# Kernel tuning notes

Hardware: AMD Instinct MI355X
Metric: run time of the kernel (lower is better)

The kernel has to match this reference:

```python
import jax, jax.numpy as jnp
import numpy as np
from jax import lax

# static config matching init_kwargs
H, W = 128, 128
THETA_RES, RHO_RES = 1.0, 1.0
C_IN, C_OUT = 64, 64
A = int(np.round(180.0 / THETA_RES))            # num angle bins = 180
R = int(np.ceil(np.sqrt(H * H + W * W) / RHO_RES))  # num rho bins = 182


def _make_rho_idx():
    # rho bin index for every (angle, pixel); pixels flattened h-major (h*W + w)
    th = np.arange(A, dtype=np.float64) * THETA_RES * np.pi / 180.0
    hh, ww = np.meshgrid(np.arange(H), np.arange(W), indexing='ij')
    xs = (ww - W / 2.0).ravel()
    ys = (hh - H / 2.0).ravel()
    r = np.round((xs[None, :] * np.cos(th)[:, None]
                  + ys[None, :] * np.sin(th)[:, None]) / RHO_RES).astype(np.int32)
    r = r + R // 2
    return np.clip(r, 0, R - 1)  # [A, H*W] int32


def dht(x, rho_idx):
    # Hough scatter: [N,C,H,W] -> [N,C,A,R]
    N, C, h, w = x.shape
    xf = x.reshape(N * C, h * w).T  # [HW, NC]

    def step(_, idx_a):
        acc = jax.ops.segment_sum(xf, idx_a, num_segments=R)  # [R, NC]
        return None, acc

    _, ht = lax.scan(step, None, rho_idx)       # [A, R, NC]
    return ht.transpose(2, 0, 1).reshape(N, C, A, R)


def idht(ht, rho_idx):
    # inverse Hough gather (transpose of dht): [N,C,A,R] -> [N,C,H,W]
    N, C, a, r = ht.shape
    hf = ht.reshape(N * C, a, r).transpose(1, 0, 2)  # [A, NC, R]

    def step(acc, args):
        ht_a, idx_a = args
        return acc + ht_a[:, idx_a], None  # gather along rho -> [NC, HW]

    acc0 = jnp.zeros((N * C, H * W), ht.dtype)
    acc, _ = lax.scan(step, acc0, (hf, rho_idx))
    return acc.reshape(N, C, H, W)


def conv91_relu(x, w, b, groups):
    # Conv2d kernel (9,1), padding (4,0), stride 1 + ReLU
    y = lax.conv_general_dilated(x, w, (1, 1), [(4, 4), (0, 0)],
                                 dimension_numbers=('NCHW', 'OIHW', 'NCHW'),
                                 feature_group_count=groups)
    return jax.nn.relu(y + b[None, :, None, None])


def setup_inputs():
    key = jax.random.key(0)
    ks = jax.random.split(key, 7)
    N = 4
    x = jax.random.normal(ks[0], (N, C_IN, H, W), dtype=jnp.float32)
    s1 = 1.0 / np.sqrt(9.0)
    s2 = 1.0 / np.sqrt(9.0 * C_IN)
    w1 = jax.random.normal(ks[1], (C_IN, 1, 9, 1), jnp.float32) * s1
    b1 = jax.random.normal(ks[2], (C_IN,), jnp.float32) * 0.01
    w2 = jax.random.normal(ks[3], (C_IN, C_IN, 9, 1), jnp.float32) * s2
    b2 = jax.random.normal(ks[4], (C_IN,), jnp.float32) * 0.01
    w3 = jax.random.normal(ks[5], (C_OUT, C_IN, 9, 1), jnp.float32) * s2
    b3 = jax.random.normal(ks[6], (C_OUT,), jnp.float32) * 0.01
    rho_idx = jnp.asarray(_make_rho_idx())  # [A, H*W] int32, precomputed buffer
    return {"x": x, "rho_idx": rho_idx, "w1": w1, "b1": b1,
            "w2": w2, "b2": b2, "w3": w3, "b3": b3}


def reference(x, rho_idx, w1, b1, w2, b2, w3, b3):
    out = dht(x, rho_idx)                       # [N,C,A,R]
    out = conv91_relu(out, w1, b1, groups=C_IN) # grouped (9,1) conv
    out = conv91_relu(out, w2, b2, groups=1)
    out = conv91_relu(out, w3, b3, groups=1)
    return idht(out, rho_idx)                   # [N,C_OUT,H,W]
```

## Files before the change

kernel.cpp:

```cpp
#include <hip/hip_runtime.h>

typedef unsigned short ushort_t;
typedef __attribute__((ext_vector_type(8))) short short8;
typedef __attribute__((ext_vector_type(4))) float float4v;

#define HW 16384
#define A_BINS 180
#define R_BINS 182
#define AP 188
#define CCH 64
#define NB 4
#define NC 256
#define MROWS (A_BINS * R_BINS)
#define MPROWS (AP * R_BINS)

static __device__ __forceinline__ float b2f(ushort_t u) {
    union { unsigned u32; float f; } c; c.u32 = ((unsigned)u) << 16; return c.f;
}
static __device__ __forceinline__ float u2f(unsigned u) {
    union { unsigned u32; float f; } c; c.u32 = u; return c.f;
}
static __device__ __forceinline__ ushort_t f2b(float f) {
    union { float f; unsigned u; } c; c.f = f;
    unsigned r = c.u + 0x7fffu + ((c.u >> 16) & 1u);
    return (ushort_t)(r >> 16);
}
static __device__ __forceinline__ float4v cvt4(uint2 u) {
    return (float4v){u2f(u.x << 16), u2f(u.x & 0xffff0000u),
                     u2f(u.y << 16), u2f(u.y & 0xffff0000u)};
}

__global__ __launch_bounds__(256) void k_transpose(const float* __restrict__ x,
                                                   ushort_t* __restrict__ xT) {
    __shared__ float tile[64][65];
    int t = threadIdx.x, lane = t & 63, g = t >> 6;
    int pBase = blockIdx.x * 64;
    int ncBase = blockIdx.y * 64;
#pragma unroll
    for (int i = 0; i < 16; ++i) {
        int ncl = g + i * 4;
        tile[ncl][lane] = x[(size_t)(ncBase + ncl) * HW + pBase + lane];
    }
    __syncthreads();
#pragma unroll
    for (int i = 0; i < 16; ++i) {
        int pl = g + i * 4;
        xT[(size_t)(pBase + pl) * 256 + ncBase + lane] = f2b(tile[lane][pl]);
    }
}

__global__ __launch_bounds__(256) void k_setup(ushort_t* __restrict__ ht0,
                                               ushort_t* __restrict__ bufA,
                                               ushort_t* __restrict__ bufB,
                                               const float* __restrict__ w2,
                                               const float* __restrict__ w3,
                                               ushort_t* __restrict__ w2b,
                                               ushort_t* __restrict__ w3b) {
    int blk = blockIdx.x, t = threadIdx.x;
    if (blk < 24) {
        int b = blk >> 3, j = blk & 7;
        int ap = (j < 4) ? j : (184 + (j - 4));
        ushort_t* base = (b == 0 ? ht0 : (b == 1 ? bufA : bufB));
        uint4* p = (uint4*)(base + (size_t)ap * (R_BINS * NC));
        int n16 = R_BINS * NC / 8;
        for (int i = t; i < n16; i += 256) p[i] = (uint4){0, 0, 0, 0};
        return;
    }
    int rep = blk - 24;
    const float* w = (rep >= 144) ? w3 : w2;
    ushort_t* wb = (rep >= 144) ? w3b : w2b;
    int idx = (rep % 144) * 256 + t;
    int j = idx & 7;
    int lane = (idx >> 3) & 63;
    int cot = (idx >> 9) & 3;
    int h = (idx >> 11) & 1;
    int k = idx >> 12;
    int co = cot * 16 + (lane & 15);
    int ci = h * 32 + (lane >> 4) * 8 + j;
    wb[idx] = f2b(w[(co * 64 + ci) * 9 + k]);
}

__global__ __launch_bounds__(256) void k_csr(const int* __restrict__ rho,
                                             int* __restrict__ offs,
                                             ushort_t* __restrict__ plist) {
    __shared__ int hist[4][R_BINS];
    __shared__ int tot[R_BINS];
    __shared__ int offl[R_BINS + 1];
    __shared__ int cur[4][R_BINS];
    __shared__ ushort_t sp[HW];
    int a = blockIdx.x, t = threadIdx.x, lane = t & 63, wv = t >> 6;
    for (int i = t; i < 4 * R_BINS; i += 256) ((int*)hist)[i] = 0;
    __syncthreads();
    const int* rA = rho + (size_t)a * HW;
#pragma unroll 4
    for (int i = 0; i < 64; ++i) {
        int r = rA[t + i * 256];
        atomicAdd(&hist[wv][r], 1);
    }
    __syncthreads();
    if (t < R_BINS) tot[t] = hist[0][t] + hist[1][t] + hist[2][t] + hist[3][t];
    __syncthreads();
    if (wv == 0) {
        int b0 = lane * 3;
        int c0 = (b0     < R_BINS) ? tot[b0]     : 0;
        int c1 = (b0 + 1 < R_BINS) ? tot[b0 + 1] : 0;
        int c2 = (b0 + 2 < R_BINS) ? tot[b0 + 2] : 0;
        int sum = c0 + c1 + c2, inc = sum;
#pragma unroll
        for (int d = 1; d < 64; d <<= 1) {
            int vv = __shfl_up(inc, d);
            if (lane >= d) inc += vv;
        }
        int excl = inc - sum;
        if (b0     < R_BINS) offl[b0]     = excl;
        if (b0 + 1 < R_BINS) offl[b0 + 1] = excl + c0;
        if (b0 + 2 < R_BINS) offl[b0 + 2] = excl + c0 + c1;
        if (lane == 63) offl[R_BINS] = inc;
    }
    __syncthreads();
    if (t < R_BINS) {
        int b = offl[t];
        cur[0][t] = b; b += hist[0][t];
        cur[1][t] = b; b += hist[1][t];
        cur[2][t] = b; b += hist[2][t];
        cur[3][t] = b;
    }
    if (t <= R_BINS) offs[a * (R_BINS + 1) + t] = offl[t];
    __syncthreads();
#pragma unroll 4
    for (int i = 0; i < 64; ++i) {
        int p = t + i * 256;
        int r = rA[p];
        int pos = atomicAdd(&cur[wv][r], 1);
        sp[pos] = (ushort_t)p;
    }
    __syncthreads();
    const uint4* spv = (const uint4*)sp;
    uint4* plv = (uint4*)(plist + (size_t)a * HW);
    for (int i = t; i < HW / 8; i += 256) plv[i] = spv[i];
}

__global__ __launch_bounds__(256, 4) void k_dht_g4(const ushort_t* __restrict__ xT,
                                                   const int* __restrict__ offs,
                                                   const ushort_t* __restrict__ plist,
                                                   ushort_t* __restrict__ ht0) {
    int ax = blockIdx.x;
    int a = ax >> 1, half = ax & 1;
    int part = blockIdx.y;
    int t = threadIdx.x, lane = t & 63, wv = t >> 6;
    int wslot = part * 4 + wv;
    int lh = lane & 31;
    bool lowhalf = (lane < 32);
    int lh4 = lh * 4;
    const ushort_t* xh = xT + half * 128;
    const uint*  plw = (const uint*)(plist + (size_t)a * HW);
    const uint4* plq = (const uint4*)plw;
    const int* offA = offs + a * (R_BINS + 1);
    size_t obase = (size_t)(a + 4) * (R_BINS * NC) + half * 128;
    for (int r = wslot; r < R_BINS; r += 64) {
        int off = __builtin_amdgcn_readfirstlane(offA[r]);
        int end = __builtin_amdgcn_readfirstlane(offA[r + 1]);
        float4v acc = (float4v){0.f, 0.f, 0.f, 0.f};
        int j = off;
        if (j < end && (j & 1)) {
            unsigned up = __builtin_amdgcn_readfirstlane(plw[j >> 1]);
            unsigned p = up >> 16;
            uint2 u = *(const uint2*)(xh + (size_t)p * 256 + lh4);
            if (lowhalf) acc += cvt4(u);
            ++j;
        }
        while (j + 2 <= end && (j & 7)) {
            unsigned w = __builtin_amdgcn_readfirstlane(plw[j >> 1]);
            unsigned pe = w & 0xffffu, po = w >> 16;
            unsigned ps = lowhalf ? pe : po;
            uint2 u = *(const uint2*)(xh + (size_t)ps * 256 + lh4);
            acc += cvt4(u);
            j += 2;
        }
        if (j + 16 <= end) {
            uint4 q0 = plq[j >> 3];
            uint4 q1 = plq[(j >> 3) + 1];
            for (; j + 16 <= end; ) {
                int jn = j + 16;
                uint4 n0, n1;
                bool more = (jn + 16 <= end);
                if (more) {
                    n0 = plq[jn >> 3];
                    n1 = plq[(jn >> 3) + 1];
                }
                unsigned w0 = __builtin_amdgcn_readfirstlane(q0.x);
                unsigned w1 = __builtin_amdgcn_readfirstlane(q0.y);
                unsigned w2 = __builtin_amdgcn_readfirstlane(q0.z);
                unsigned w3 = __builtin_amdgcn_readfirstlane(q0.w);
                unsigned w4 = __builtin_amdgcn_readfirstlane(q1.x);
                unsigned w5 = __builtin_amdgcn_readfirstlane(q1.y);
                unsigned w6 = __builtin_amdgcn_readfirstlane(q1.z);
                unsigned w7 = __builtin_amdgcn_readfirstlane(q1.w);
                unsigned s0 = lowhalf ? (w0 & 0xffffu) : (w0 >> 16);
                unsigned s1 = lowhalf ? (w1 & 0xffffu) : (w1 >> 16);
                unsigned s2 = lowhalf ? (w2 & 0xffffu) : (w2 >> 16);
                unsigned s3 = lowhalf ? (w3 & 0xffffu) : (w3 >> 16);
                unsigned s4 = lowhalf ? (w4 & 0xffffu) : (w4 >> 16);
                unsigned s5 = lowhalf ? (w5 & 0xffffu) : (w5 >> 16);
                unsigned s6 = lowhalf ? (w6 & 0xffffu) : (w6 >> 16);
                unsigned s7 = lowhalf ? (w7 & 0xffffu) : (w7 >> 16);
                uint2 u0 = *(const uint2*)(xh + (size_t)s0 * 256 + lh4);
                uint2 u1 = *(const uint2*)(xh + (size_t)s1 * 256 + lh4);
                uint2 u2 = *(const uint2*)(xh + (size_t)s2 * 256 + lh4);
                uint2 u3 = *(const uint2*)(xh + (size_t)s3 * 256 + lh4);
                uint2 u4 = *(const uint2*)(xh + (size_t)s4 * 256 + lh4);
                uint2 u5 = *(const uint2*)(xh + (size_t)s5 * 256 + lh4);
                uint2 u6 = *(const uint2*)(xh + (size_t)s6 * 256 + lh4);
                uint2 u7 = *(const uint2*)(xh + (size_t)s7 * 256 + lh4);
                acc += cvt4(u0); acc += cvt4(u1); acc += cvt4(u2); acc += cvt4(u3);
                acc += cvt4(u4); acc += cvt4(u5); acc += cvt4(u6); acc += cvt4(u7);
                q0 = n0; q1 = n1; j = jn;
            }
        }
        for (; j + 8 <= end; j += 8) {
            uint4 q = plq[j >> 3];
            unsigned w0 = __builtin_amdgcn_readfirstlane(q.x);
            unsigned w1 = __builtin_amdgcn_readfirstlane(q.y);
            unsigned w2 = __builtin_amdgcn_readfirstlane(q.z);
            unsigned w3 = __builtin_amdgcn_readfirstlane(q.w);
            unsigned s0 = lowhalf ? (w0 & 0xffffu) : (w0 >> 16);
            unsigned s1 = lowhalf ? (w1 & 0xffffu) : (w1 >> 16);
            unsigned s2 = lowhalf ? (w2 & 0xffffu) : (w2 >> 16);
            unsigned s3 = lowhalf ? (w3 & 0xffffu) : (w3 >> 16);
            uint2 u0 = *(const uint2*)(xh + (size_t)s0 * 256 + lh4);
            uint2 u1 = *(const uint2*)(xh + (size_t)s1 * 256 + lh4);
            uint2 u2 = *(const uint2*)(xh + (size_t)s2 * 256 + lh4);
            uint2 u3 = *(const uint2*)(xh + (size_t)s3 * 256 + lh4);
            acc += cvt4(u0); acc += cvt4(u1); acc += cvt4(u2); acc += cvt4(u3);
        }
        while (j + 2 <= end) {
            unsigned w = __builtin_amdgcn_readfirstlane(plw[j >> 1]);
            unsigned pe = w & 0xffffu, po = w >> 16;
            unsigned ps = lowhalf ? pe : po;
            uint2 u = *(const uint2*)(xh + (size_t)ps * 256 + lh4);
            acc += cvt4(u);
            j += 2;
        }
        if (j < end) {
            unsigned up = __builtin_amdgcn_readfirstlane(plw[j >> 1]);
            unsigned p = up & 0xffffu;
            uint2 u = *(const uint2*)(xh + (size_t)p * 256 + lh4);
            if (lowhalf) acc += cvt4(u);
        }
        float4v oth;
        oth.x = __shfl(acc.x, lane ^ 32);
        oth.y = __shfl(acc.y, lane ^ 32);
        oth.z = __shfl(acc.z, lane ^ 32);
        oth.w = __shfl(acc.w, lane ^ 32);
        acc += oth;
        if (lowhalf) {
            unsigned lo = (unsigned)f2b(acc.x) | ((unsigned)f2b(acc.y) << 16);
            unsigned hi = (unsigned)f2b(acc.z) | ((unsigned)f2b(acc.w) << 16);
            *(uint2*)(ht0 + obase + (size_t)r * NC + lh4) = (uint2){lo, hi};
        }
    }
}

__global__ __launch_bounds__(256) void k_conv1(const ushort_t* __restrict__ ht0,
                                               const float* __restrict__ w1,
                                               const float* __restrict__ b1,
                                               ushort_t* __restrict__ bufA) {
    int t = threadIdx.x, c = t & 63;
    int r = blockIdx.x;
    int a0 = blockIdx.y * 30;
    float wr[9];
#pragma unroll
    for (int k = 0; k < 9; ++k) wr[k] = w1[c * 9 + k];
    float bb = b1[c];
    const ushort_t* ip = ht0 + ((size_t)a0 * R_BINS + r) * NC + t;
    float v[38];
#pragma unroll
    for (int j = 0; j < 38; ++j) v[j] = b2f(ip[(size_t)j * (R_BINS * NC)]);
    ushort_t* op = bufA + ((size_t)(a0 + 4) * R_BINS + r) * NC + t;
#pragma unroll
    for (int i = 0; i < 30; ++i) {
        float s = bb;
#pragma unroll
        for (int k = 0; k < 9; ++k) s = fmaf(v[i + k], wr[k], s);
        op[(size_t)i * (R_BINS * NC)] = f2b(fmaxf(s, 0.f));
    }
}

__global__ __launch_bounds__(256) void k_gemm(const ushort_t* __restrict__ in,
                                              const ushort_t* __restrict__ wb,
                                              const float* __restrict__ bias,
                                              ushort_t* __restrict__ out,
                                              int outRowOff) {
    __shared__ ushort_t Bs[36864];
    int t = threadIdx.x, lane = t & 63, wv = t >> 6;
    {
        const uint4* src = (const uint4*)wb;
        uint4* dst = (uint4*)Bs;
        for (int i = t; i < 36864 / 8; i += 256) dst[i] = src[i];
    }
    __syncthreads();
    int m = lane & 15, q = lane >> 4;
    int n = blockIdx.y;
    int rowBase = blockIdx.x * 256 + wv * 64;
    const ushort_t* inN = in + n * 64;
    size_t rof[4];
#pragma unroll
    for (int tl = 0; tl < 4; ++tl) {
        int row = rowBase + tl * 16 + m;
        int rowc = row < MROWS ? row : (MROWS - 1);
        rof[tl] = (size_t)rowc * NC;
    }
    float4v acc[4][4];
#pragma unroll
    for (int tl = 0; tl < 4; ++tl)
#pragma unroll
        for (int i = 0; i < 4; ++i) acc[tl][i] = (float4v){0.f, 0.f, 0.f, 0.f};

#pragma unroll
    for (int k = 0; k < 9; ++k) {
#pragma unroll
        for (int h = 0; h < 2; ++h) {
            const ushort_t* base = inN + (size_t)k * (R_BINS * NC) + h * 32 + q * 8;
            short8 af0 = *(const short8*)(base + rof[0]);
            short8 af1 = *(const short8*)(base + rof[1]);
            short8 af2 = *(const short8*)(base + rof[2]);
            short8 af3 = *(const short8*)(base + rof[3]);
            const ushort_t* bl = Bs + (size_t)((k * 2 + h) * 4) * 512 + lane * 8;
            short8 b0 = *(const short8*)(bl);
            short8 b1v = *(const short8*)(bl + 512);
            short8 b2v = *(const short8*)(bl + 1024);
            short8 b3v = *(const short8*)(bl + 1536);
            acc[0][0] = __builtin_amdgcn_mfma_f32_16x16x32_bf16(af0, b0, acc[0][0], 0, 0, 0);
            acc[0][1] = __builtin_amdgcn_mfma_f32_16x16x32_bf16(af0, b1v, acc[0][1], 0, 0, 0);
            acc[0][2] = __builtin_amdgcn_mfma_f32_16x16x32_bf16(af0, b2v, acc[0][2], 0, 0, 0);
            acc[0][3] = __builtin_amdgcn_mfma_f32_16x16x32_bf16(af0, b3v, acc[0][3], 0, 0, 0);
            acc[1][0] = __builtin_amdgcn_mfma_f32_16x16x32_bf16(af1, b0, acc[1][0], 0, 0, 0);
            acc[1][1] = __builtin_amdgcn_mfma_f32_16x16x32_bf16(af1, b1v, acc[1][1], 0, 0, 0);
            acc[1][2] = __builtin_amdgcn_mfma_f32_16x16x32_bf16(af1, b2v, acc[1][2], 0, 0, 0);
            acc[1][3] = __builtin_amdgcn_mfma_f32_16x16x32_bf16(af1, b3v, acc[1][3], 0, 0, 0);
            acc[2][0] = __builtin_amdgcn_mfma_f32_16x16x32_bf16(af2, b0, acc[2][0], 0, 0, 0);
            acc[2][1] = __builtin_amdgcn_mfma_f32_16x16x32_bf16(af2, b1v, acc[2][1], 0, 0, 0);
            acc[2][2] = __builtin_amdgcn_mfma_f32_16x16x32_bf16(af2, b2v, acc[2][2], 0, 0, 0);
            acc[2][3] = __builtin_amdgcn_mfma_f32_16x16x32_bf16(af2, b3v, acc[2][3], 0, 0, 0);
            acc[3][0] = __builtin_amdgcn_mfma_f32_16x16x32_bf16(af3, b0, acc[3][0], 0, 0, 0);
            acc[3][1] = __builtin_amdgcn_mfma_f32_16x16x32_bf16(af3, b1v, acc[3][1], 0, 0, 0);
            acc[3][2] = __builtin_amdgcn_mfma_f32_16x16x32_bf16(af3, b2v, acc[3][2], 0, 0, 0);
            acc[3][3] = __builtin_amdgcn_mfma_f32_16x16x32_bf16(af3, b3v, acc[3][3], 0, 0, 0);
        }
    }

    ushort_t* outN = out + n * 64;
#pragma unroll
    for (int tl = 0; tl < 4; ++tl) {
#pragma unroll
        for (int cot = 0; cot < 4; ++cot) {
            int co = cot * 16 + m;
            float bv = bias[co];
#pragma unroll
            for (int i = 0; i < 4; ++i) {
                int rowD = rowBase + tl * 16 + q * 4 + i;
                float v = fmaxf(acc[tl][cot][i] + bv, 0.f);
                if (rowD < MROWS) outN[(size_t)(rowD + outRowOff) * NC + co] = f2b(v);
            }
        }
    }
}

union SharedIdht {
    int rhoL[A_BINS * 32];
    float tile[2 * 256 * 33];
};

#define IDHT_LOAD(S, ang) do { \
    int4 rv0_ = *(const int4*)&u.rhoL[(ang) * 32 + wq * 8]; \
    int4 rv1_ = *(const int4*)&u.rhoL[(ang) * 32 + wq * 8 + 4]; \
    int rrs_[8] = {rv0_.x, rv0_.y, rv0_.z, rv0_.w, rv1_.x, rv1_.y, rv1_.z, rv1_.w}; \
    const ushort_t* bA_ = buf3 + (size_t)(ang) * (R_BINS * NC); \
    _Pragma("unroll") \
    for (int i_ = 0; i_ < 8; ++i_) { \
        int r_ = __builtin_amdgcn_readfirstlane(rrs_[i_]); \
        S[i_] = *(const uint2*)(bA_ + (size_t)r_ * NC + lo4); \
    } } while (0)

#define IDHT_CONSUME(S) do { \
    _Pragma("unroll") \
    for (int i_ = 0; i_ < 8; ++i_) accv[i_] += cvt4(S[i_]); \
    } while (0)

__global__ __launch_bounds__(512, 2) void k_idht(const ushort_t* __restrict__ buf3,
                                                 const int* __restrict__ rho,
                                                 float* __restrict__ outp) {
    __shared__ SharedIdht u;
    int t = threadIdx.x, lane = t & 63, wv = t >> 6;
    int grp = wv >> 2;
    int wq = wv & 3;
    int P0 = blockIdx.x * 32;
    int lo4 = lane << 2;
    for (int i = t; i < A_BINS * 32; i += 512) {
        int a = i >> 5, px = i & 31;
        u.rhoL[a * 32 + px] = rho[(size_t)a * HW + P0 + px];
    }
    __syncthreads();
    float4v accv[8];
#pragma unroll
    for (int i = 0; i < 8; ++i) accv[i] = (float4v){0.f, 0.f, 0.f, 0.f};
    int a0 = grp * 90;

    uint2 S0[8], S1[8], S2[8];
    IDHT_LOAD(S0, a0);
    IDHT_LOAD(S1, a0 + 1);
    IDHT_LOAD(S2, a0 + 2);
    for (int k = 0; k <= 84; k += 3) {
        IDHT_CONSUME(S0); IDHT_LOAD(S0, a0 + k + 3);
        IDHT_CONSUME(S1); IDHT_LOAD(S1, a0 + k + 4);
        IDHT_CONSUME(S2); IDHT_LOAD(S2, a0 + k + 5);
    }
    IDHT_CONSUME(S0);
    IDHT_CONSUME(S1);
    IDHT_CONSUME(S2);

    __syncthreads();
#pragma unroll
    for (int i = 0; i < 8; ++i) {
        int px = wq * 8 + i;
#pragma unroll
        for (int c = 0; c < 4; ++c)
            u.tile[(size_t)grp * 8448 + (lane * 4 + c) * 33 + px] = accv[i][c];
    }
    __syncthreads();
    int px = t & 31, nc0 = t >> 5;
    float* on = outp + P0 + px;
#pragma unroll
    for (int k = 0; k < 16; ++k) {
        int nc = nc0 + k * 16;
        on[(size_t)nc * HW] = u.tile[nc * 33 + px] + u.tile[8448 + nc * 33 + px];
    }
}

extern "C" void kernel_launch(void* const* d_in, const int* in_sizes, int n_in,
                              void* d_out, int out_size, void* d_ws, size_t ws_size,
                              hipStream_t stream) {
    const float* x   = (const float*)d_in[0];
    const int*   rho = (const int*)d_in[1];
    const float* w1  = (const float*)d_in[2];
    const float* b1  = (const float*)d_in[3];
    const float* w2  = (const float*)d_in[4];
    const float* b2  = (const float*)d_in[5];
    const float* w3  = (const float*)d_in[6];
    const float* b3  = (const float*)d_in[7];
    float* outp = (float*)d_out;

    char* ws = (char*)d_ws;
    size_t off = 0;
    auto alloc = [&](size_t bytes) -> void* {
        void* p = ws + off;
        off = (off + bytes + 255) & ~(size_t)255;
        return p;
    };
    ushort_t* xT    = (ushort_t*)alloc((size_t)HW * NC * 2);
    ushort_t* ht0   = (ushort_t*)alloc((size_t)AP * R_BINS * NC * 2);
    ushort_t* bufA  = (ushort_t*)alloc((size_t)AP * R_BINS * NC * 2);
    ushort_t* bufB  = (ushort_t*)alloc((size_t)AP * R_BINS * NC * 2);
    ushort_t* buf3  = (ushort_t*)alloc((size_t)A_BINS * R_BINS * NC * 2);
    ushort_t* w2b   = (ushort_t*)alloc(36864 * 2);
    ushort_t* w3b   = (ushort_t*)alloc(36864 * 2);
    int*      offs  = (int*)alloc((size_t)A_BINS * (R_BINS + 1) * 4);
    ushort_t* plist = (ushort_t*)alloc((size_t)A_BINS * HW * 2);

    k_transpose<<<dim3(256, 4), 256, 0, stream>>>(x, xT);
    k_setup<<<312, 256, 0, stream>>>(ht0, bufA, bufB, w2, w3, w2b, w3b);
    k_csr<<<A_BINS, 256, 0, stream>>>(rho, offs, plist);
    k_dht_g4<<<dim3(360, 16), 256, 0, stream>>>(xT, offs, plist, ht0);
    k_conv1<<<dim3(R_BINS, 6), 256, 0, stream>>>(ht0, w1, b1, bufA);
    k_gemm<<<dim3(128, NB), 256, 0, stream>>>(bufA, w2b, b2, bufB, 728);
    k_gemm<<<dim3(128, NB), 256, 0, stream>>>(bufB, w3b, b3, buf3, 0);
    k_idht<<<dim3(512), 512, 0, stream>>>(buf3, rho, outp);
}
```

Measured before the change: 371.5 us.

## Pad CSR segments to multiples of eight and widen DHT/IDHT gathers to 16-byte loads

The CSR pixel lists now pad each rho segment to a multiple of eight entries, using a dummy zero pixel row appended to the transposed input. This removes the misaligned head and tail loops in the DHT. The DHT gather now has each wave process four pixels per step with 16-byte loads per lane, followed by a cross-lane shuffle reduction. The IDHT likewise loads 16 bytes per lane covering two pixels per wave half. The padding adds some wasted gathers of the zero row, and the plist stride grows to 17664 entries.

Measured after the change: 315.9 us. 15.0% less time.

```diff
diff --git a/kernel.cpp b/kernel.cpp
--- a/kernel.cpp
+++ b/kernel.cpp
@@ -13,6 +13,8 @@
 #define NC 256
 #define MROWS (A_BINS * R_BINS)
 #define MPROWS (AP * R_BINS)
+#define PADPX HW
+#define PLSTRIDE 17664
 
 static __device__ __forceinline__ float b2f(ushort_t u) {
     union { unsigned u32; float f; } c; c.u32 = ((unsigned)u) << 16; return c.f;
@@ -55,8 +57,13 @@
                                                const float* __restrict__ w2,
                                                const float* __restrict__ w3,
                                                ushort_t* __restrict__ w2b,
-                                               ushort_t* __restrict__ w3b) {
+                                               ushort_t* __restrict__ w3b,
+                                               ushort_t* __restrict__ xT) {
     int blk = blockIdx.x, t = threadIdx.x;
+    if (blk == 312) {
+        if (t < 64) ((uint2*)(xT + (size_t)PADPX * NC))[t] = (uint2){0u, 0u};
+        return;
+    }
     if (blk < 24) {
         int b = blk >> 3, j = blk & 7;
         int ap = (j < 4) ? j : (184 + (j - 4));
@@ -87,7 +94,7 @@
     __shared__ int tot[R_BINS];
     __shared__ int offl[R_BINS + 1];
     __shared__ int cur[4][R_BINS];
-    __shared__ ushort_t sp[HW];
+    __shared__ ushort_t sp[PLSTRIDE];
     int a = blockIdx.x, t = threadIdx.x, lane = t & 63, wv = t >> 6;
     for (int i = t; i < 4 * R_BINS; i += 256) ((int*)hist)[i] = 0;
     __syncthreads();
@@ -102,9 +109,9 @@
     __syncthreads();
     if (wv == 0) {
         int b0 = lane * 3;
-        int c0 = (b0     < R_BINS) ? tot[b0]     : 0;
-        int c1 = (b0 + 1 < R_BINS) ? tot[b0 + 1] : 0;
-        int c2 = (b0 + 2 < R_BINS) ? tot[b0 + 2] : 0;
+        int c0 = (b0     < R_BINS) ? ((tot[b0]     + 7) & ~7) : 0;
+        int c1 = (b0 + 1 < R_BINS) ? ((tot[b0 + 1] + 7) & ~7) : 0;
+        int c2 = (b0 + 2 < R_BINS) ? ((tot[b0 + 2] + 7) & ~7) : 0;
         int sum = c0 + c1 + c2, inc = sum;
 #pragma unroll
         for (int d = 1; d < 64; d <<= 1) {
@@ -135,12 +142,19 @@
         sp[pos] = (ushort_t)p;
     }
     __syncthreads();
+    if (t < R_BINS) {
+        int base = offl[t] + tot[t];
+        int pend = offl[t + 1];
+        for (int k = base; k < pend; ++k) sp[k] = (ushort_t)PADPX;
+    }
+    __syncthreads();
+    int len = offl[R_BINS];
     const uint4* spv = (const uint4*)sp;
-    uint4* plv = (uint4*)(plist + (size_t)a * HW);
-    for (int i = t; i < HW / 8; i += 256) plv[i] = spv[i];
-}
-
-__global__ __launch_bounds__(256, 4) void k_dht_g4(const ushort_t* __restrict__ xT,
+    uint4* plv = (uint4*)(plist + (size_t)a * PLSTRIDE);
+    for (int i = t; i < len / 8; i += 256) plv[i] = spv[i];
+}
+
+__global__ __launch_bounds__(256, 4) void k_dht_g5(const ushort_t* __restrict__ xT,
                                                    const int* __restrict__ offs,
                                                    const ushort_t* __restrict__ plist,
                                                    ushort_t* __restrict__ ht0) {
@@ -149,114 +163,61 @@
     int part = blockIdx.y;
     int t = threadIdx.x, lane = t & 63, wv = t >> 6;
     int wslot = part * 4 + wv;
-    int lh = lane & 31;
-    bool lowhalf = (lane < 32);
-    int lh4 = lh * 4;
-    const ushort_t* xh = xT + half * 128;
-    const uint*  plw = (const uint*)(plist + (size_t)a * HW);
-    const uint4* plq = (const uint4*)plw;
+    int nl = lane & 15;
+    unsigned lhb = (unsigned)nl * 16;
+    unsigned shsel = (lane & 16) ? 16u : 0u;
+    const char* xh = (const char*)xT + half * 256;
+    const uint4* plq = (const uint4*)(plist + (size_t)a * PLSTRIDE);
     const int* offA = offs + a * (R_BINS + 1);
     size_t obase = (size_t)(a + 4) * (R_BINS * NC) + half * 128;
     for (int r = wslot; r < R_BINS; r += 64) {
         int off = __builtin_amdgcn_readfirstlane(offA[r]);
         int end = __builtin_amdgcn_readfirstlane(offA[r + 1]);
-        float4v acc = (float4v){0.f, 0.f, 0.f, 0.f};
+        float4v acc0 = (float4v){0.f, 0.f, 0.f, 0.f};
+        float4v acc1 = (float4v){0.f, 0.f, 0.f, 0.f};
         int j = off;
-        if (j < end && (j & 1)) {
-            unsigned up = __builtin_amdgcn_readfirstlane(plw[j >> 1]);
-            unsigned p = up >> 16;
-            uint2 u = *(const uint2*)(xh + (size_t)p * 256 + lh4);
-            if (lowhalf) acc += cvt4(u);
-            ++j;
-        }
-        while (j + 2 <= end && (j & 7)) {
-            unsigned w = __builtin_amdgcn_readfirstlane(plw[j >> 1]);
-            unsigned pe = w & 0xffffu, po = w >> 16;
-            unsigned ps = lowhalf ? pe : po;
-            uint2 u = *(const uint2*)(xh + (size_t)ps * 256 + lh4);
-            acc += cvt4(u);
-            j += 2;
-        }
-        if (j + 16 <= end) {
-            uint4 q0 = plq[j >> 3];
-            uint4 q1 = plq[(j >> 3) + 1];
-            for (; j + 16 <= end; ) {
-                int jn = j + 16;
-                uint4 n0, n1;
-                bool more = (jn + 16 <= end);
-                if (more) {
-                    n0 = plq[jn >> 3];
-                    n1 = plq[(jn >> 3) + 1];
+        if (j < end) {
+            uint4 w = plq[j >> 3];
+            for (;;) {
+                int jn = j + 8;
+                uint4 wn = (uint4){0u, 0u, 0u, 0u};
+                bool more = jn < end;
+                if (more) wn = plq[jn >> 3];
+                {
+                    unsigned we = (lane & 32) ? w.y : w.x;
+                    unsigned ps = (we >> shsel) & 0xffffu;
+                    uint4 u = *(const uint4*)(xh + ((size_t)ps << 9) + lhb);
+                    acc0 += cvt4((uint2){u.x, u.y});
+                    acc1 += cvt4((uint2){u.z, u.w});
                 }
-                unsigned w0 = __builtin_amdgcn_readfirstlane(q0.x);
-                unsigned w1 = __builtin_amdgcn_readfirstlane(q0.y);
-                unsigned w2 = __builtin_amdgcn_readfirstlane(q0.z);
-                unsigned w3 = __builtin_amdgcn_readfirstlane(q0.w);
-                unsigned w4 = __builtin_amdgcn_readfirstlane(q1.x);
-                unsigned w5 = __builtin_amdgcn_readfirstlane(q1.y);
-                unsigned w6 = __builtin_amdgcn_readfirstlane(q1.z);
-                unsigned w7 = __builtin_amdgcn_readfirstlane(q1.w);
-                unsigned s0 = lowhalf ? (w0 & 0xffffu) : (w0 >> 16);
-                unsigned s1 = lowhalf ? (w1 & 0xffffu) : (w1 >> 16);
-                unsigned s2 = lowhalf ? (w2 & 0xffffu) : (w2 >> 16);
-                unsigned s3 = lowhalf ? (w3 & 0xffffu) : (w3 >> 16);
-                unsigned s4 = lowhalf ? (w4 & 0xffffu) : (w4 >> 16);
-                unsigned s5 = lowhalf ? (w5 & 0xffffu) : (w5 >> 16);
-                unsigned s6 = lowhalf ? (w6 & 0xffffu) : (w6 >> 16);
-                unsigned s7 = lowhalf ? (w7 & 0xffffu) : (w7 >> 16);
-                uint2 u0 = *(const uint2*)(xh + (size_t)s0 * 256 + lh4);
-                uint2 u1 = *(const uint2*)(xh + (size_t)s1 * 256 + lh4);
-                uint2 u2 = *(const uint2*)(xh + (size_t)s2 * 256 + lh4);
-                uint2 u3 = *(const uint2*)(xh + (size_t)s3 * 256 + lh4);
-                uint2 u4 = *(const uint2*)(xh + (size_t)s4 * 256 + lh4);
-                uint2 u5 = *(const uint2*)(xh + (size_t)s5 * 256 + lh4);
-                uint2 u6 = *(const uint2*)(xh + (size_t)s6 * 256 + lh4);
-                uint2 u7 = *(const uint2*)(xh + (size_t)s7 * 256 + lh4);
-                acc += cvt4(u0); acc += cvt4(u1); acc += cvt4(u2); acc += cvt4(u3);
-                acc += cvt4(u4); acc += cvt4(u5); acc += cvt4(u6); acc += cvt4(u7);
-                q0 = n0; q1 = n1; j = jn;
+                {
+                    unsigned we = (lane & 32) ? w.w : w.z;
+                    unsigned ps = (we >> shsel) & 0xffffu;
+                    uint4 u = *(const uint4*)(xh + ((size_t)ps << 9) + lhb);
+                    acc0 += cvt4((uint2){u.x, u.y});
+                    acc1 += cvt4((uint2){u.z, u.w});
+                }
+                if (!more) break;
+                w = wn; j = jn;
             }
         }
-        for (; j + 8 <= end; j += 8) {
-            uint4 q = plq[j >> 3];
-            unsigned w0 = __builtin_amdgcn_readfirstlane(q.x);
-            unsigned w1 = __builtin_amdgcn_readfirstlane(q.y);
-            unsigned w2 = __builtin_amdgcn_readfirstlane(q.z);
-            unsigned w3 = __builtin_amdgcn_readfirstlane(q.w);
-            unsigned s0 = lowhalf ? (w0 & 0xffffu) : (w0 >> 16);
-            unsigned s1 = lowhalf ? (w1 & 0xffffu) : (w1 >> 16);
-            unsigned s2 = lowhalf ? (w2 & 0xffffu) : (w2 >> 16);
-            unsigned s3 = lowhalf ? (w3 & 0xffffu) : (w3 >> 16);
-            uint2 u0 = *(const uint2*)(xh + (size_t)s0 * 256 + lh4);
-            uint2 u1 = *(const uint2*)(xh + (size_t)s1 * 256 + lh4);
-            uint2 u2 = *(const uint2*)(xh + (size_t)s2 * 256 + lh4);
-            uint2 u3 = *(const uint2*)(xh + (size_t)s3 * 256 + lh4);
-            acc += cvt4(u0); acc += cvt4(u1); acc += cvt4(u2); acc += cvt4(u3);
-        }
-        while (j + 2 <= end) {
-            unsigned w = __builtin_amdgcn_readfirstlane(plw[j >> 1]);
-            unsigned pe = w & 0xffffu, po = w >> 16;
-            unsigned ps = lowhalf ? pe : po;
-            uint2 u = *(const uint2*)(xh + (size_t)ps * 256 + lh4);
-            acc += cvt4(u);
-            j += 2;
-        }
-        if (j < end) {
-            unsigned up = __builtin_amdgcn_readfirstlane(plw[j >> 1]);
-            unsigned p = up & 0xffffu;
-            uint2 u = *(const uint2*)(xh + (size_t)p * 256 + lh4);
-            if (lowhalf) acc += cvt4(u);
-        }
-        float4v oth;
-        oth.x = __shfl(acc.x, lane ^ 32);
-        oth.y = __shfl(acc.y, lane ^ 32);
-        oth.z = __shfl(acc.z, lane ^ 32);
-        oth.w = __shfl(acc.w, lane ^ 32);
-        acc += oth;
-        if (lowhalf) {
-            unsigned lo = (unsigned)f2b(acc.x) | ((unsigned)f2b(acc.y) << 16);
-            unsigned hi = (unsigned)f2b(acc.z) | ((unsigned)f2b(acc.w) << 16);
-            *(uint2*)(ht0 + obase + (size_t)r * NC + lh4) = (uint2){lo, hi};
+#pragma unroll
+        for (int c = 0; c < 4; ++c) {
+            acc0[c] += __shfl_xor(acc0[c], 16);
+            acc1[c] += __shfl_xor(acc1[c], 16);
+        }
+#pragma unroll
+        for (int c = 0; c < 4; ++c) {
+            acc0[c] += __shfl_xor(acc0[c], 32);
+            acc1[c] += __shfl_xor(acc1[c], 32);
+        }
+        if (lane < 16) {
+            uint4 o;
+            o.x = (unsigned)f2b(acc0[0]) | ((unsigned)f2b(acc0[1]) << 16);
+            o.y = (unsigned)f2b(acc0[2]) | ((unsigned)f2b(acc0[3]) << 16);
+            o.z = (unsigned)f2b(acc1[0]) | ((unsigned)f2b(acc1[1]) << 16);
+            o.w = (unsigned)f2b(acc1[2]) | ((unsigned)f2b(acc1[3]) << 16);
+            *(uint4*)(ht0 + obase + (size_t)r * NC + nl * 8) = o;
         }
     }
 }
@@ -374,18 +335,19 @@
 #define IDHT_LOAD(S, ang) do { \
     int4 rv0_ = *(const int4*)&u.rhoL[(ang) * 32 + wq * 8]; \
     int4 rv1_ = *(const int4*)&u.rhoL[(ang) * 32 + wq * 8 + 4]; \
-    int rrs_[8] = {rv0_.x, rv0_.y, rv0_.z, rv0_.w, rv1_.x, rv1_.y, rv1_.z, rv1_.w}; \
-    const ushort_t* bA_ = buf3 + (size_t)(ang) * (R_BINS * NC); \
-    _Pragma("unroll") \
-    for (int i_ = 0; i_ < 8; ++i_) { \
-        int r_ = __builtin_amdgcn_readfirstlane(rrs_[i_]); \
-        S[i_] = *(const uint2*)(bA_ + (size_t)r_ * NC + lo4); \
-    } } while (0)
+    const char* bA_ = (const char*)buf3 + (size_t)(ang) * (R_BINS * NC * 2); \
+    { unsigned r_ = (unsigned)(h ? rv0_.y : rv0_.x); S[0] = *(const uint4*)(bA_ + ((size_t)r_ << 9) + lhb); } \
+    { unsigned r_ = (unsigned)(h ? rv0_.w : rv0_.z); S[1] = *(const uint4*)(bA_ + ((size_t)r_ << 9) + lhb); } \
+    { unsigned r_ = (unsigned)(h ? rv1_.y : rv1_.x); S[2] = *(const uint4*)(bA_ + ((size_t)r_ << 9) + lhb); } \
+    { unsigned r_ = (unsigned)(h ? rv1_.w : rv1_.z); S[3] = *(const uint4*)(bA_ + ((size_t)r_ << 9) + lhb); } \
+    } while (0)
 
 #define IDHT_CONSUME(S) do { \
     _Pragma("unroll") \
-    for (int i_ = 0; i_ < 8; ++i_) accv[i_] += cvt4(S[i_]); \
-    } while (0)
+    for (int p_ = 0; p_ < 4; ++p_) { \
+        accv[2 * p_]     += cvt4((uint2){S[p_].x, S[p_].y}); \
+        accv[2 * p_ + 1] += cvt4((uint2){S[p_].z, S[p_].w}); \
+    } } while (0)
 
 __global__ __launch_bounds__(512, 2) void k_idht(const ushort_t* __restrict__ buf3,
                                                  const int* __restrict__ rho,
@@ -395,7 +357,8 @@
     int grp = wv >> 2;
     int wq = wv & 3;
     int P0 = blockIdx.x * 32;
-    int lo4 = lane << 2;
+    int h = lane >> 5;
+    unsigned lhb = (unsigned)(lane & 31) * 16;
     for (int i = t; i < A_BINS * 32; i += 512) {
         int a = i >> 5, px = i & 31;
         u.rhoL[a * 32 + px] = rho[(size_t)a * HW + P0 + px];
@@ -406,7 +369,7 @@
     for (int i = 0; i < 8; ++i) accv[i] = (float4v){0.f, 0.f, 0.f, 0.f};
     int a0 = grp * 90;
 
-    uint2 S0[8], S1[8], S2[8];
+    uint4 S0[4], S1[4], S2[4];
     IDHT_LOAD(S0, a0);
     IDHT_LOAD(S1, a0 + 1);
     IDHT_LOAD(S2, a0 + 2);
@@ -421,11 +384,12 @@
 
     __syncthreads();
 #pragma unroll
-    for (int i = 0; i < 8; ++i) {
-        int px = wq * 8 + i;
-#pragma unroll
-        for (int c = 0; c < 4; ++c)
-            u.tile[(size_t)grp * 8448 + (lane * 4 + c) * 33 + px] = accv[i][c];
+    for (int p = 0; p < 4; ++p) {
+        int px = wq * 8 + p * 2 + h;
+#pragma unroll
+        for (int cc = 0; cc < 8; ++cc)
+            u.tile[(size_t)grp * 8448 + ((lane & 31) * 8 + cc) * 33 + px] =
+                accv[2 * p + (cc >> 2)][cc & 3];
     }
     __syncthreads();
     int px = t & 31, nc0 = t >> 5;
@@ -457,7 +421,7 @@
         off = (off + bytes + 255) & ~(size_t)255;
         return p;
     };
-    ushort_t* xT    = (ushort_t*)alloc((size_t)HW * NC * 2);
+    ushort_t* xT    = (ushort_t*)alloc((size_t)(HW + 8) * NC * 2);
     ushort_t* ht0   = (ushort_t*)alloc((size_t)AP * R_BINS * NC * 2);
     ushort_t* bufA  = (ushort_t*)alloc((size_t)AP * R_BINS * NC * 2);
     ushort_t* bufB  = (ushort_t*)alloc((size_t)AP * R_BINS * NC * 2);
@@ -465,12 +429,12 @@
     ushort_t* w2b   = (ushort_t*)alloc(36864 * 2);
     ushort_t* w3b   = (ushort_t*)alloc(36864 * 2);
     int*      offs  = (int*)alloc((size_t)A_BINS * (R_BINS + 1) * 4);
-    ushort_t* plist = (ushort_t*)alloc((size_t)A_BINS * HW * 2);
+    ushort_t* plist = (ushort_t*)alloc((size_t)A_BINS * PLSTRIDE * 2);
 
     k_transpose<<<dim3(256, 4), 256, 0, stream>>>(x, xT);
-    k_setup<<<312, 256, 0, stream>>>(ht0, bufA, bufB, w2, w3, w2b, w3b);
+    k_setup<<<313, 256, 0, stream>>>(ht0, bufA, bufB, w2, w3, w2b, w3b, xT);
     k_csr<<<A_BINS, 256, 0, stream>>>(rho, offs, plist);
-    k_dht_g4<<<dim3(360, 16), 256, 0, stream>>>(xT, offs, plist, ht0);
+    k_dht_g5<<<dim3(360, 16), 256, 0, stream>>>(xT, offs, plist, ht0);
     k_conv1<<<dim3(R_BINS, 6), 256, 0, stream>>>(ht0, w1, b1, bufA);
     k_gemm<<<dim3(128, NB), 256, 0, stream>>>(bufA, w2b, b2, bufB, 728);
     k_gemm<<<dim3(128, NB), 256, 0, stream>>>(bufB, w3b, b3, buf3, 0);
```
